# Kernel tuning notes

Measured on AMD Instinct MI355X. Metric: run time of the kernel, lower is better.

The kernel has to match this reference:

```python
import jax, jax.numpy as jnp
import numpy as np

B, K = 4, 128
V_IN, V_OUT = 256, 256
E_IN, E_OUT = 512, 512
P_PE, T_PE = 200, 100
HEADS = 16  # c_atten_head


def _lin(key, din, dout):
    kw, kb = jax.random.split(key)
    W = jax.random.normal(kw, (din, dout), jnp.float32) / np.sqrt(din).astype(np.float32)
    b = jax.random.normal(kb, (dout,), jnp.float32) * 0.01
    return W, b


def setup_inputs() -> dict:
    key = jax.random.key(0)
    ks = jax.random.split(key, 14)
    v_f = jax.random.normal(ks[0], (B, K, V_IN), jnp.float32)
    e_f = jax.random.normal(ks[1], (B, K * K, E_IN), jnp.float32)
    p_pe = jax.random.normal(ks[2], (B, K, P_PE), jnp.float32)
    t_pe = jax.random.normal(ks[3], (B, T_PE), jnp.float32)
    e_agg_mask = (jax.random.uniform(ks[4], (B, K, K)) > 0.1).astype(jnp.float32)
    v_agg_mask = (jax.random.uniform(ks[5], (B, K)) > 0.1).astype(jnp.float32)
    W_vpe, b_vpe = _lin(ks[6], V_IN + P_PE + T_PE, V_IN)
    W_epe, b_epe = _lin(ks[7], E_IN + T_PE, E_IN)
    W_ev1, b_ev1 = _lin(ks[8], E_IN + 2 * V_IN, E_OUT)
    W_ev2, b_ev2 = _lin(ks[9], E_OUT, E_OUT)
    W_q, b_q = _lin(ks[10], V_IN, E_OUT)
    W_k, b_k = _lin(ks[11], V_IN, E_OUT)
    W_self, b_self = _lin(ks[12], V_IN, E_OUT)
    W_out, b_out = _lin(ks[13], 2 * E_OUT, V_OUT)
    return dict(v_f=v_f, e_f=e_f, p_pe=p_pe, t_pe=t_pe,
                e_agg_mask=e_agg_mask, v_agg_mask=v_agg_mask,
                W_vpe=W_vpe, b_vpe=b_vpe, W_epe=W_epe, b_epe=b_epe,
                W_ev1=W_ev1, b_ev1=b_ev1, W_ev2=W_ev2, b_ev2=b_ev2,
                W_q=W_q, b_q=b_q, W_k=W_k, b_k=b_k,
                W_self=W_self, b_self=b_self, W_out=W_out, b_out=b_out)


def reference(v_f, e_f, p_pe, t_pe, e_agg_mask, v_agg_mask,
              W_vpe, b_vpe, W_epe, b_epe, W_ev1, b_ev1, W_ev2, b_ev2,
              W_q, b_q, W_k, b_k, W_self, b_self, W_out, b_out):
    silu = jax.nn.silu
    # PE binding
    t_v = jnp.broadcast_to(t_pe[:, None, :], (B, K, T_PE))
    v = silu(jnp.concatenate([v_f, p_pe, t_v], -1) @ W_vpe + b_vpe)          # (B,K,V_IN)
    t_e = jnp.broadcast_to(t_pe[:, None, :], (B, K * K, T_PE))
    e = silu(jnp.concatenate([e_f, t_e], -1) @ W_epe + b_epe)                # (B,K*K,E_IN)
    # dense all-pairs node features -> edge values
    pair = jnp.concatenate([jnp.broadcast_to(v[:, :, None, :], (B, K, K, V_IN)),
                            jnp.broadcast_to(v[:, None, :, :], (B, K, K, V_IN))], -1)
    ev_in = jnp.concatenate([pair.reshape(B, K * K, 2 * V_IN), e], -1)
    e_value = silu(ev_in @ W_ev1 + b_ev1) @ W_ev2 + b_ev2                     # (B,K*K,E_OUT)
    agg_e = e_value.reshape(B, K, K, E_OUT)
    # elementwise-multiply / head-sum attention
    q = v @ W_q + b_q                                                         # (B,K,E_OUT)
    k = v @ W_k + b_k
    att = (q[:, :, None, :] * k[:, None, :, :]).reshape(B, K, K, E_OUT // HEADS, HEADS)
    att = att.sum(-1, keepdims=True) / np.float32(np.sqrt(HEADS * 3.0))       # (B,K,K,G,1)
    a = jax.nn.sigmoid(att) * e_agg_mask[..., None, None]
    a = a / (a.sum(2, keepdims=True) + 1e-6)
    a = jnp.broadcast_to(a, (B, K, K, E_OUT // HEADS, HEADS)).reshape(B, K, K, E_OUT)
    agg_v = (a * agg_e).sum(2)                                                # (B,K,E_OUT)
    v2 = agg_v + silu(v @ W_self + b_self)
    # masked max-pool over nodes
    pooled = (v2 - 1e9 * (1.0 - v_agg_mask)[..., None]).max(1, keepdims=True)
    pooled = jnp.broadcast_to(pooled, (B, K, E_OUT))
    v_out = silu(jnp.concatenate([v2, pooled], -1) @ W_out + b_out)           # (B,K,V_OUT)
    return v_out, e_value
```

## Files before the change

kernel.cpp:

```cpp
#include <hip/hip_runtime.h>

typedef unsigned short ushort_t;
typedef __attribute__((ext_vector_type(8))) short bf16x8;
typedef __attribute__((ext_vector_type(4))) float f32x4;

__device__ __forceinline__ ushort_t f2bf(float f) {
    union { float f; unsigned u; } v; v.f = f;
    unsigned r = v.u + 0x7FFFu + ((v.u >> 16) & 1u);
    return (ushort_t)(r >> 16);
}
__device__ __forceinline__ float siluf(float x) { return x / (1.f + __expf(-x)); }
__device__ __forceinline__ float sigm(float x)  { return 1.f / (1.f + __expf(-x)); }

__device__ __forceinline__ void gl2lds16(const void* g, void* l) {
    __builtin_amdgcn_global_load_lds(
        (__attribute__((address_space(1))) void*)(const_cast<void*>(g)),
        (__attribute__((address_space(3))) void*)(l), 16, 0, 0);
}


__global__ void k_prep(const float* t_pe, const float* W_vpe, const float* b_vpe,
                       const float* W_epe, const float* b_epe,
                       float* c_v, float* c_e) {
    int b = blockIdx.x, t = threadIdx.x;
    {
        float acc = b_epe[t];
        for (int u = 0; u < 100; ++u) acc += t_pe[b*100+u] * W_epe[(512+u)*512 + t];
        c_e[b*512 + t] = acc;
    }
    if (t < 256) {
        float acc = b_vpe[t];
        for (int u = 0; u < 100; ++u) acc += t_pe[b*100+u] * W_vpe[(456+u)*256 + t];
        c_v[b*256 + t] = acc;
    }
}

__global__ void k_transpose(const float* W_epe, const float* W_ev1, const float* W_ev2,
                            ushort_t* WT_epe, ushort_t* WT_c, ushort_t* WT_ev2) {
    int n = blockIdx.x;
    int mat = blockIdx.y;
    const float* src; ushort_t* dst;
    if (mat == 0)      { src = W_epe;            dst = WT_epe; }
    else if (mat == 1) { src = W_ev1 + 512*512;  dst = WT_c;   }
    else               { src = W_ev2;            dst = WT_ev2; }
    for (int k = threadIdx.x; k < 512; k += 256)
        dst[n*512 + k] = f2bf(src[k*512 + n]);
}

__global__ void k_node_v(const float* v_f, const float* p_pe, const float* W_vpe,
                         const float* c_v, float* v) {
    __shared__ float rv[4][256];
    __shared__ float rp[4][200];
    int r0 = blockIdx.x * 4, t = threadIdx.x;
    for (int rr = 0; rr < 4; ++rr) {
        rv[rr][t] = v_f[(r0+rr)*256 + t];
        if (t < 200) rp[rr][t] = p_pe[(r0+rr)*200 + t];
    }
    __syncthreads();
    int b = r0 >> 7;
    float acc[4];
    float cv = c_v[b*256 + t];
    for (int rr = 0; rr < 4; ++rr) acc[rr] = cv;
    for (int k = 0; k < 256; ++k) {
        float w = W_vpe[k*256 + t];
        #pragma unroll
        for (int rr = 0; rr < 4; ++rr) acc[rr] += rv[rr][k] * w;
    }
    for (int k = 0; k < 200; ++k) {
        float w = W_vpe[(256+k)*256 + t];
        #pragma unroll
        for (int rr = 0; rr < 4; ++rr) acc[rr] += rp[rr][k] * w;
    }
    for (int rr = 0; rr < 4; ++rr) v[(r0+rr)*256 + t] = siluf(acc[rr]);
}

__global__ void k_node_proj(const float* v,
                            const float* W_q, const float* b_q,
                            const float* W_k, const float* b_k,
                            const float* W_self, const float* b_self,
                            const float* W_ev1, const float* b_ev1,
                            float* q, float* kk, float* vs, float* P, float* Q) {
    __shared__ float rv[4][256];
    int r0 = blockIdx.x * 4, which = blockIdx.y, t = threadIdx.x;
    for (int rr = 0; rr < 4; ++rr) rv[rr][t] = v[(r0+rr)*256 + t];
    __syncthreads();
    const float* W; const float* bias = nullptr; float* out; bool do_silu = false;
    if (which == 0)      { W = W_q;    bias = b_q;    out = q;  }
    else if (which == 1) { W = W_k;    bias = b_k;    out = kk; }
    else if (which == 2) { W = W_self; bias = b_self; out = vs; do_silu = true; }
    else if (which == 3) { W = W_ev1;  bias = b_ev1;  out = P;  }
    else                 { W = W_ev1 + 256*512;       out = Q;  }
    float acc[4][2] = {};
    for (int k = 0; k < 256; ++k) {
        float w0 = W[k*512 + t];
        float w1 = W[k*512 + t + 256];
        #pragma unroll
        for (int rr = 0; rr < 4; ++rr) {
            acc[rr][0] += rv[rr][k] * w0;
            acc[rr][1] += rv[rr][k] * w1;
        }
    }
    float bb0 = bias ? bias[t] : 0.f;
    float bb1 = bias ? bias[t + 256] : 0.f;
    for (int rr = 0; rr < 4; ++rr) {
        float x0 = acc[rr][0] + bb0;
        float x1 = acc[rr][1] + bb1;
        if (do_silu) { x0 = siluf(x0); x1 = siluf(x1); }
        out[(r0+rr)*512 + t]       = x0;
        out[(r0+rr)*512 + t + 256] = x1;
    }
}


__global__ __launch_bounds__(256) void k_gemm1(const float* Ef, const ushort_t* BT,
                                               const float* c_e, ushort_t* Eout) {
    __shared__ __align__(16) ushort_t As[128*40];
    __shared__ __align__(16) ushort_t Bs[128*32];
    int m0 = blockIdx.x * 128, n0 = blockIdx.y * 128;
    int t = threadIdx.x;
    int wv = t >> 6, lane = t & 63;
    int wm = (wv >> 1) * 64, wn = (wv & 1) * 64;
    int ml = lane & 15, quad = lane >> 4;
    f32x4 acc[4][4] = {};

    int arow = t >> 1, acol = (t & 1) * 16;
    const float* gA = Ef + (size_t)(m0 + arow) * 512 + acol;
    int brow = t >> 2, bseg = t & 3;
    const ushort_t* gB0 = BT + (size_t)(n0 + brow) * 512 + bseg * 8;
    const ushort_t* gB1 = BT + (size_t)(n0 + 64 + brow) * 512 + bseg * 8;
    ushort_t* lB0 = Bs + wv * 512;
    ushort_t* lB1 = Bs + 2048 + wv * 512;

    for (int kk = 0; kk < 512; kk += 32) {
        gl2lds16(gB0 + kk, lB0);
        gl2lds16(gB1 + kk, lB1);
        const float* ga = gA + kk;
        float4 f0 = *(const float4*)(ga);
        float4 f1 = *(const float4*)(ga + 4);
        float4 f2 = *(const float4*)(ga + 8);
        float4 f3 = *(const float4*)(ga + 12);
        ushort_t* d = As + arow * 40 + acol;
        ((ushort4*)d)[0] = make_ushort4(f2bf(f0.x), f2bf(f0.y), f2bf(f0.z), f2bf(f0.w));
        ((ushort4*)d)[1] = make_ushort4(f2bf(f1.x), f2bf(f1.y), f2bf(f1.z), f2bf(f1.w));
        ((ushort4*)d)[2] = make_ushort4(f2bf(f2.x), f2bf(f2.y), f2bf(f2.z), f2bf(f2.w));
        ((ushort4*)d)[3] = make_ushort4(f2bf(f3.x), f2bf(f3.y), f2bf(f3.z), f2bf(f3.w));
        __syncthreads();
        bf16x8 a[4], b[4];
        #pragma unroll
        for (int tm = 0; tm < 4; ++tm)
            a[tm] = *(const bf16x8*)(As + (wm + tm*16 + ml) * 40 + quad * 8);
        #pragma unroll
        for (int tn = 0; tn < 4; ++tn)
            b[tn] = *(const bf16x8*)(Bs + (wn + tn*16 + ml) * 32 + quad * 8);
        #pragma unroll
        for (int tm = 0; tm < 4; ++tm)
            #pragma unroll
            for (int tn = 0; tn < 4; ++tn)
                acc[tm][tn] = __builtin_amdgcn_mfma_f32_16x16x32_bf16(a[tm], b[tn], acc[tm][tn], 0, 0, 0);
        __syncthreads();
    }
    #pragma unroll
    for (int tm = 0; tm < 4; ++tm)
        #pragma unroll
        for (int tn = 0; tn < 4; ++tn)
            #pragma unroll
            for (int r = 0; r < 4; ++r) {
                int gm = m0 + wm + tm*16 + quad*4 + r;
                int gn = n0 + wn + tn*16 + ml;
                float x = acc[tm][tn][r] + c_e[(gm >> 14)*512 + gn];
                Eout[(size_t)gm*512 + gn] = f2bf(siluf(x));
            }
}

template <int MODE>
__global__ __launch_bounds__(256) void k_gemm_b(const ushort_t* A, const ushort_t* BT,
                                                const float* x0, const float* x1,
                                                ushort_t* out16, float* out32) {
    __shared__ __align__(16) ushort_t As[128*32];
    __shared__ __align__(16) ushort_t Bs[128*32];
    int m0 = blockIdx.x * 128, n0 = blockIdx.y * 128;
    int t = threadIdx.x;
    int wv = t >> 6, lane = t & 63;
    int wm = (wv >> 1) * 64, wn = (wv & 1) * 64;
    int ml = lane & 15, quad = lane >> 4;
    f32x4 acc[4][4] = {};

    int srow = t >> 2, sseg = t & 3;
    const ushort_t* gA0 = A + (size_t)(m0 + srow) * 512 + sseg * 8;
    const ushort_t* gA1 = A + (size_t)(m0 + 64 + srow) * 512 + sseg * 8;
    const ushort_t* gB0 = BT + (size_t)(n0 + srow) * 512 + sseg * 8;
    const ushort_t* gB1 = BT + (size_t)(n0 + 64 + srow) * 512 + sseg * 8;
    ushort_t* lA0 = As + wv * 512;
    ushort_t* lA1 = As + 2048 + wv * 512;
    ushort_t* lB0 = Bs + wv * 512;
    ushort_t* lB1 = Bs + 2048 + wv * 512;

    for (int kk = 0; kk < 512; kk += 32) {
        gl2lds16(gA0 + kk, lA0);
        gl2lds16(gA1 + kk, lA1);
        gl2lds16(gB0 + kk, lB0);
        gl2lds16(gB1 + kk, lB1);
        __syncthreads();
        bf16x8 a[4], b[4];
        #pragma unroll
        for (int tm = 0; tm < 4; ++tm)
            a[tm] = *(const bf16x8*)(As + (wm + tm*16 + ml) * 32 + quad * 8);
        #pragma unroll
        for (int tn = 0; tn < 4; ++tn)
            b[tn] = *(const bf16x8*)(Bs + (wn + tn*16 + ml) * 32 + quad * 8);
        #pragma unroll
        for (int tm = 0; tm < 4; ++tm)
            #pragma unroll
            for (int tn = 0; tn < 4; ++tn)
                acc[tm][tn] = __builtin_amdgcn_mfma_f32_16x16x32_bf16(a[tm], b[tn], acc[tm][tn], 0, 0, 0);
        __syncthreads();
    }
    #pragma unroll
    for (int tm = 0; tm < 4; ++tm)
        #pragma unroll
        for (int tn = 0; tn < 4; ++tn)
            #pragma unroll
            for (int r = 0; r < 4; ++r) {
                int gm = m0 + wm + tm*16 + quad*4 + r;
                int gn = n0 + wn + tn*16 + ml;
                float x = acc[tm][tn][r];
                if (MODE == 0) {
                    int b_ = gm >> 14, ij = gm & 16383, i = ij >> 7, j = ij & 127;
                    x += x0[(size_t)((b_ << 7) + i) * 512 + gn] + x1[(size_t)((b_ << 7) + j) * 512 + gn];
                    out16[(size_t)gm*512 + gn] = f2bf(siluf(x));
                } else {
                    x += x0[gn];
                    out32[(size_t)gm*512 + gn] = x;
                }
            }
}

__global__ __launch_bounds__(256) void k_attn(const float* q, const float* kmat,
                                              const float* emask, const float* evalue,
                                              const float* vs, float* v2) {
    int bi = blockIdx.x; int b = bi >> 7, i = bi & 127;
    int t = threadIdx.x;
    __shared__ __align__(16) float qrow[512];
    __shared__ float s[128][33];
    __shared__ float invd[32];
    qrow[t]       = q[(size_t)bi*512 + t];
    qrow[t + 256] = q[(size_t)bi*512 + t + 256];
    __syncthreads();
    {
        int j = t >> 1, g0 = (t & 1) * 16;
        const float* kr = kmat + ((size_t)b*128 + j) * 512;
        float msk = emask[(size_t)b*16384 + i*128 + j];
        for (int gg = 0; gg < 16; ++gg) {
            int g = g0 + gg;
            const float4* k4 = (const float4*)(kr + g*16);
            const float4* q4 = (const float4*)(qrow + g*16);
            float acc = 0.f;
            #pragma unroll
            for (int c = 0; c < 4; ++c) {
                float4 kv = k4[c], qv = q4[c];
                acc += kv.x*qv.x + kv.y*qv.y + kv.z*qv.z + kv.w*qv.w;
            }
            s[j][g] = sigm(acc * 0.14433756729740645f) * msk;
        }
    }
    __syncthreads();
    if (t < 32) {
        float d = 1e-6f;
        for (int j = 0; j < 128; ++j) d += s[j][t];
        invd[t] = 1.f / d;
    }
    __syncthreads();
    int d0 = t * 2;
    int g = d0 >> 4;
    float a0 = 0.f, a1 = 0.f;
    const float* ev = evalue + ((size_t)b*16384 + i*128) * 512 + d0;
    for (int j = 0; j < 128; ++j) {
        float aw = s[j][g];
        float2 e2 = *(const float2*)(ev + (size_t)j * 512);
        a0 += aw * e2.x; a1 += aw * e2.y;
    }
    float iv = invd[g];
    size_t o = (size_t)bi*512 + d0;
    v2[o]     = a0 * iv + vs[o];
    v2[o + 1] = a1 * iv + vs[o + 1];
}

__global__ void k_pool(const float* v2, const float* vmask, const float* W_out,
                       const float* b_out, float* cpool) {
    int b = blockIdx.x, t = threadIdx.x;
    __shared__ float pooled[512];
    for (int d = t; d < 512; d += 256) {
        float m = -1e30f;
        for (int i = 0; i < 128; ++i) {
            float val = v2[((size_t)(b*128 + i))*512 + d] - 1e9f * (1.f - vmask[b*128 + i]);
            m = fmaxf(m, val);
        }
        pooled[d] = m;
    }
    __syncthreads();
    float acc = b_out[t];
    for (int d = 0; d < 512; ++d) acc += pooled[d] * W_out[(512 + d)*256 + t];
    cpool[b*256 + t] = acc;
}

__global__ void k_node_out(const float* v2, const float* W_out, const float* cpool,
                           float* out) {
    __shared__ float rv[4][512];
    int r0 = blockIdx.x * 4, t = threadIdx.x;
    for (int rr = 0; rr < 4; ++rr) {
        rv[rr][t]       = v2[(size_t)(r0+rr)*512 + t];
        rv[rr][t + 256] = v2[(size_t)(r0+rr)*512 + t + 256];
    }
    __syncthreads();
    int b = r0 >> 7;
    float acc[4];
    float cp = cpool[b*256 + t];
    for (int rr = 0; rr < 4; ++rr) acc[rr] = cp;
    for (int k = 0; k < 512; ++k) {
        float w = W_out[k*256 + t];
        #pragma unroll
        for (int rr = 0; rr < 4; ++rr) acc[rr] += rv[rr][k] * w;
    }
    for (int rr = 0; rr < 4; ++rr) out[(r0+rr)*256 + t] = siluf(acc[rr]);
}

extern "C" void kernel_launch(void* const* d_in, const int* in_sizes, int n_in,
                              void* d_out, int out_size, void* d_ws, size_t ws_size,
                              hipStream_t stream) {
    const float* v_f    = (const float*)d_in[0];
    const float* e_f    = (const float*)d_in[1];
    const float* p_pe   = (const float*)d_in[2];
    const float* t_pe   = (const float*)d_in[3];
    const float* emask  = (const float*)d_in[4];
    const float* vmask  = (const float*)d_in[5];
    const float* W_vpe  = (const float*)d_in[6];
    const float* b_vpe  = (const float*)d_in[7];
    const float* W_epe  = (const float*)d_in[8];
    const float* b_epe  = (const float*)d_in[9];
    const float* W_ev1  = (const float*)d_in[10];
    const float* b_ev1  = (const float*)d_in[11];
    const float* W_ev2  = (const float*)d_in[12];
    const float* b_ev2  = (const float*)d_in[13];
    const float* W_q    = (const float*)d_in[14];
    const float* b_q    = (const float*)d_in[15];
    const float* W_k    = (const float*)d_in[16];
    const float* b_k    = (const float*)d_in[17];
    const float* W_self = (const float*)d_in[18];
    const float* b_self = (const float*)d_in[19];
    const float* W_out  = (const float*)d_in[20];
    const float* b_out  = (const float*)d_in[21];

    float* out_v = (float*)d_out;
    float* out_e = (float*)d_out + 131072;

    char* w = (char*)d_ws;
    ushort_t* WT_epe = (ushort_t*)w; w += 512*512*2;
    ushort_t* WT_c   = (ushort_t*)w; w += 512*512*2;
    ushort_t* WT_ev2 = (ushort_t*)w; w += 512*512*2;
    float* c_v   = (float*)w; w += 4*256*4;
    float* c_e   = (float*)w; w += 4*512*4;
    float* v     = (float*)w; w += 512*256*4;
    float* qbuf  = (float*)w; w += 512*512*4;
    float* kbuf  = (float*)w; w += 512*512*4;
    float* vsbuf = (float*)w; w += 512*512*4;
    float* Pbuf  = (float*)w; w += 512*512*4;
    float* Qbuf  = (float*)w; w += 512*512*4;
    float* v2buf = (float*)w; w += 512*512*4;
    float* cpool = (float*)w; w += 4*256*4;
    ushort_t* e16 = (ushort_t*)w; w += (size_t)65536*512*2;
    ushort_t* h16 = (ushort_t*)w; w += (size_t)65536*512*2;

    k_prep<<<4, 512, 0, stream>>>(t_pe, W_vpe, b_vpe, W_epe, b_epe, c_v, c_e);
    k_transpose<<<dim3(512, 3), 256, 0, stream>>>(W_epe, W_ev1, W_ev2, WT_epe, WT_c, WT_ev2);
    k_node_v<<<128, 256, 0, stream>>>(v_f, p_pe, W_vpe, c_v, v);
    k_node_proj<<<dim3(128, 5), 256, 0, stream>>>(v, W_q, b_q, W_k, b_k, W_self, b_self,
                                                  W_ev1, b_ev1, qbuf, kbuf, vsbuf, Pbuf, Qbuf);
    k_gemm1<<<dim3(512, 4), 256, 0, stream>>>(e_f, WT_epe, c_e, e16);
    k_gemm_b<0><<<dim3(512, 4), 256, 0, stream>>>(e16, WT_c, Pbuf, Qbuf, h16, nullptr);
    k_gemm_b<1><<<dim3(512, 4), 256, 0, stream>>>(h16, WT_ev2, b_ev2, nullptr, nullptr, out_e);
    k_attn<<<512, 256, 0, stream>>>(qbuf, kbuf, emask, out_e, vsbuf, v2buf);
    k_pool<<<4, 256, 0, stream>>>(v2buf, vmask, W_out, b_out, cpool);
    k_node_out<<<128, 256, 0, stream>>>(v2buf, W_out, cpool, out_v);
}
```

Before: 689.1 us.

## Fuse attention aggregation into final edge GEMM epilogue and pre-convert e_f to bf16

Splits attention into a weight-only kernel that writes normalized per-(i,j,group) weights, then folds the weighted sum over j into the epilogue of the last edge GEMM. Each 128-row tile there covers exactly one (b,i) node, so the fp32 e_value no longer has to be re-read from memory. The first GEMM now takes a bf16 copy of e_f made by a separate conversion pass instead of converting inside the main loop, and tiles are remapped by XCD index for L2 locality. The cost is the extra conversion pass, an anorm buffer, and shuffle reductions in the epilogue.

```diff
diff --git a/kernel.cpp b/kernel.cpp
--- a/kernel.cpp
+++ b/kernel.cpp
@@ -47,6 +47,15 @@
         dst[n*512 + k] = f2bf(src[k*512 + n]);
 }
 
+__global__ __launch_bounds__(256) void k_cvt(const float* src, ushort_t* dst) {
+    size_t id = (size_t)blockIdx.x * 256 + threadIdx.x;
+    const float4* s = (const float4*)src + id * 2;
+    float4 a = s[0], b = s[1];
+    ushort4* d = (ushort4*)dst + id * 2;
+    d[0] = make_ushort4(f2bf(a.x), f2bf(a.y), f2bf(a.z), f2bf(a.w));
+    d[1] = make_ushort4(f2bf(b.x), f2bf(b.y), f2bf(b.z), f2bf(b.w));
+}
+
 __global__ void k_node_v(const float* v_f, const float* p_pe, const float* W_vpe,
                          const float* c_v, float* v) {
     __shared__ float rv[4][256];
@@ -111,133 +120,8 @@
     }
 }
 
-
-__global__ __launch_bounds__(256) void k_gemm1(const float* Ef, const ushort_t* BT,
-                                               const float* c_e, ushort_t* Eout) {
-    __shared__ __align__(16) ushort_t As[128*40];
-    __shared__ __align__(16) ushort_t Bs[128*32];
-    int m0 = blockIdx.x * 128, n0 = blockIdx.y * 128;
-    int t = threadIdx.x;
-    int wv = t >> 6, lane = t & 63;
-    int wm = (wv >> 1) * 64, wn = (wv & 1) * 64;
-    int ml = lane & 15, quad = lane >> 4;
-    f32x4 acc[4][4] = {};
-
-    int arow = t >> 1, acol = (t & 1) * 16;
-    const float* gA = Ef + (size_t)(m0 + arow) * 512 + acol;
-    int brow = t >> 2, bseg = t & 3;
-    const ushort_t* gB0 = BT + (size_t)(n0 + brow) * 512 + bseg * 8;
-    const ushort_t* gB1 = BT + (size_t)(n0 + 64 + brow) * 512 + bseg * 8;
-    ushort_t* lB0 = Bs + wv * 512;
-    ushort_t* lB1 = Bs + 2048 + wv * 512;
-
-    for (int kk = 0; kk < 512; kk += 32) {
-        gl2lds16(gB0 + kk, lB0);
-        gl2lds16(gB1 + kk, lB1);
-        const float* ga = gA + kk;
-        float4 f0 = *(const float4*)(ga);
-        float4 f1 = *(const float4*)(ga + 4);
-        float4 f2 = *(const float4*)(ga + 8);
-        float4 f3 = *(const float4*)(ga + 12);
-        ushort_t* d = As + arow * 40 + acol;
-        ((ushort4*)d)[0] = make_ushort4(f2bf(f0.x), f2bf(f0.y), f2bf(f0.z), f2bf(f0.w));
-        ((ushort4*)d)[1] = make_ushort4(f2bf(f1.x), f2bf(f1.y), f2bf(f1.z), f2bf(f1.w));
-        ((ushort4*)d)[2] = make_ushort4(f2bf(f2.x), f2bf(f2.y), f2bf(f2.z), f2bf(f2.w));
-        ((ushort4*)d)[3] = make_ushort4(f2bf(f3.x), f2bf(f3.y), f2bf(f3.z), f2bf(f3.w));
-        __syncthreads();
-        bf16x8 a[4], b[4];
-        #pragma unroll
-        for (int tm = 0; tm < 4; ++tm)
-            a[tm] = *(const bf16x8*)(As + (wm + tm*16 + ml) * 40 + quad * 8);
-        #pragma unroll
-        for (int tn = 0; tn < 4; ++tn)
-            b[tn] = *(const bf16x8*)(Bs + (wn + tn*16 + ml) * 32 + quad * 8);
-        #pragma unroll
-        for (int tm = 0; tm < 4; ++tm)
-            #pragma unroll
-            for (int tn = 0; tn < 4; ++tn)
-                acc[tm][tn] = __builtin_amdgcn_mfma_f32_16x16x32_bf16(a[tm], b[tn], acc[tm][tn], 0, 0, 0);
-        __syncthreads();
-    }
-    #pragma unroll
-    for (int tm = 0; tm < 4; ++tm)
-        #pragma unroll
-        for (int tn = 0; tn < 4; ++tn)
-            #pragma unroll
-            for (int r = 0; r < 4; ++r) {
-                int gm = m0 + wm + tm*16 + quad*4 + r;
-                int gn = n0 + wn + tn*16 + ml;
-                float x = acc[tm][tn][r] + c_e[(gm >> 14)*512 + gn];
-                Eout[(size_t)gm*512 + gn] = f2bf(siluf(x));
-            }
-}
-
-template <int MODE>
-__global__ __launch_bounds__(256) void k_gemm_b(const ushort_t* A, const ushort_t* BT,
-                                                const float* x0, const float* x1,
-                                                ushort_t* out16, float* out32) {
-    __shared__ __align__(16) ushort_t As[128*32];
-    __shared__ __align__(16) ushort_t Bs[128*32];
-    int m0 = blockIdx.x * 128, n0 = blockIdx.y * 128;
-    int t = threadIdx.x;
-    int wv = t >> 6, lane = t & 63;
-    int wm = (wv >> 1) * 64, wn = (wv & 1) * 64;
-    int ml = lane & 15, quad = lane >> 4;
-    f32x4 acc[4][4] = {};
-
-    int srow = t >> 2, sseg = t & 3;
-    const ushort_t* gA0 = A + (size_t)(m0 + srow) * 512 + sseg * 8;
-    const ushort_t* gA1 = A + (size_t)(m0 + 64 + srow) * 512 + sseg * 8;
-    const ushort_t* gB0 = BT + (size_t)(n0 + srow) * 512 + sseg * 8;
-    const ushort_t* gB1 = BT + (size_t)(n0 + 64 + srow) * 512 + sseg * 8;
-    ushort_t* lA0 = As + wv * 512;
-    ushort_t* lA1 = As + 2048 + wv * 512;
-    ushort_t* lB0 = Bs + wv * 512;
-    ushort_t* lB1 = Bs + 2048 + wv * 512;
-
-    for (int kk = 0; kk < 512; kk += 32) {
-        gl2lds16(gA0 + kk, lA0);
-        gl2lds16(gA1 + kk, lA1);
-        gl2lds16(gB0 + kk, lB0);
-        gl2lds16(gB1 + kk, lB1);
-        __syncthreads();
-        bf16x8 a[4], b[4];
-        #pragma unroll
-        for (int tm = 0; tm < 4; ++tm)
-            a[tm] = *(const bf16x8*)(As + (wm + tm*16 + ml) * 32 + quad * 8);
-        #pragma unroll
-        for (int tn = 0; tn < 4; ++tn)
-            b[tn] = *(const bf16x8*)(Bs + (wn + tn*16 + ml) * 32 + quad * 8);
-        #pragma unroll
-        for (int tm = 0; tm < 4; ++tm)
-            #pragma unroll
-            for (int tn = 0; tn < 4; ++tn)
-                acc[tm][tn] = __builtin_amdgcn_mfma_f32_16x16x32_bf16(a[tm], b[tn], acc[tm][tn], 0, 0, 0);
-        __syncthreads();
-    }
-    #pragma unroll
-    for (int tm = 0; tm < 4; ++tm)
-        #pragma unroll
-        for (int tn = 0; tn < 4; ++tn)
-            #pragma unroll
-            for (int r = 0; r < 4; ++r) {
-                int gm = m0 + wm + tm*16 + quad*4 + r;
-                int gn = n0 + wn + tn*16 + ml;
-                float x = acc[tm][tn][r];
-                if (MODE == 0) {
-                    int b_ = gm >> 14, ij = gm & 16383, i = ij >> 7, j = ij & 127;
-                    x += x0[(size_t)((b_ << 7) + i) * 512 + gn] + x1[(size_t)((b_ << 7) + j) * 512 + gn];
-                    out16[(size_t)gm*512 + gn] = f2bf(siluf(x));
-                } else {
-                    x += x0[gn];
-                    out32[(size_t)gm*512 + gn] = x;
-                }
-            }
-}
-
-__global__ __launch_bounds__(256) void k_attn(const float* q, const float* kmat,
-                                              const float* emask, const float* evalue,
-                                              const float* vs, float* v2) {
+__global__ __launch_bounds__(256) void k_attw(const float* q, const float* kmat,
+                                              const float* emask, float* anorm) {
     int bi = blockIdx.x; int b = bi >> 7, i = bi & 127;
     int t = threadIdx.x;
     __shared__ __align__(16) float qrow[512];
@@ -270,19 +154,120 @@
         invd[t] = 1.f / d;
     }
     __syncthreads();
-    int d0 = t * 2;
-    int g = d0 >> 4;
-    float a0 = 0.f, a1 = 0.f;
-    const float* ev = evalue + ((size_t)b*16384 + i*128) * 512 + d0;
-    for (int j = 0; j < 128; ++j) {
-        float aw = s[j][g];
-        float2 e2 = *(const float2*)(ev + (size_t)j * 512);
-        a0 += aw * e2.x; a1 += aw * e2.y;
-    }
-    float iv = invd[g];
-    size_t o = (size_t)bi*512 + d0;
-    v2[o]     = a0 * iv + vs[o];
-    v2[o + 1] = a1 * iv + vs[o + 1];
+    float* dst = anorm + (size_t)bi * 4096;
+    for (int idx = t; idx < 4096; idx += 256) {
+        int j = idx >> 5, g = idx & 31;
+        dst[idx] = s[j][g] * invd[g];
+    }
+}
+
+template <int MODE>
+__global__ __launch_bounds__(256) void k_gemm(const ushort_t* A, const ushort_t* BT,
+                                              const float* e0, const float* e1,
+                                              const float* e2,
+                                              ushort_t* out16, float* out32,
+                                              float* v2out) {
+    __shared__ __align__(16) ushort_t As[128*32];
+    __shared__ __align__(16) ushort_t Bs[128*32];
+    __shared__ float aw[(MODE == 2) ? 4096 : 4];
+    __shared__ float red[(MODE == 2) ? 256 : 4];
+
+    int lin = blockIdx.x;
+    int xcd = lin & 7, idx = lin >> 3;
+    int mt = xcd * 64 + (idx >> 2);
+    int nt = idx & 3;
+    int m0 = mt * 128, n0 = nt * 128;
+    int t = threadIdx.x;
+    int wv = t >> 6, lane = t & 63;
+    int wm = (wv >> 1) * 64, wn = (wv & 1) * 64;
+    int ml = lane & 15, quad = lane >> 4;
+    f32x4 acc[4][4] = {};
+
+    if (MODE == 2) {
+        const float4* src = (const float4*)(e1 + (size_t)mt * 4096);
+        float4* dst = (float4*)aw;
+        for (int i = t; i < 1024; i += 256) dst[i] = src[i];
+    }
+
+    int srow = t >> 2, sseg = t & 3;
+    const ushort_t* gA0 = A + (size_t)(m0 + srow) * 512 + sseg * 8;
+    const ushort_t* gA1 = A + (size_t)(m0 + 64 + srow) * 512 + sseg * 8;
+    const ushort_t* gB0 = BT + (size_t)(n0 + srow) * 512 + sseg * 8;
+    const ushort_t* gB1 = BT + (size_t)(n0 + 64 + srow) * 512 + sseg * 8;
+    ushort_t* lA0 = As + wv * 512;
+    ushort_t* lA1 = As + 2048 + wv * 512;
+    ushort_t* lB0 = Bs + wv * 512;
+    ushort_t* lB1 = Bs + 2048 + wv * 512;
+
+    for (int kk = 0; kk < 512; kk += 32) {
+        gl2lds16(gA0 + kk, lA0);
+        gl2lds16(gA1 + kk, lA1);
+        gl2lds16(gB0 + kk, lB0);
+        gl2lds16(gB1 + kk, lB1);
+        __syncthreads();
+        bf16x8 a[4], b[4];
+        #pragma unroll
+        for (int tm = 0; tm < 4; ++tm)
+            a[tm] = *(const bf16x8*)(As + (wm + tm*16 + ml) * 32 + quad * 8);
+        #pragma unroll
+        for (int tn = 0; tn < 4; ++tn)
+            b[tn] = *(const bf16x8*)(Bs + (wn + tn*16 + ml) * 32 + quad * 8);
+        #pragma unroll
+        for (int tm = 0; tm < 4; ++tm)
+            #pragma unroll
+            for (int tn = 0; tn < 4; ++tn)
+                acc[tm][tn] = __builtin_amdgcn_mfma_f32_16x16x32_bf16(a[tm], b[tn], acc[tm][tn], 0, 0, 0);
+        __syncthreads();
+    }
+
+    if (MODE == 2) {
+        float partial[4] = {0.f, 0.f, 0.f, 0.f};
+        #pragma unroll
+        for (int tm = 0; tm < 4; ++tm)
+            #pragma unroll
+            for (int tn = 0; tn < 4; ++tn)
+                #pragma unroll
+                for (int r = 0; r < 4; ++r) {
+                    int j  = wm + tm*16 + quad*4 + r;
+                    int gn = n0 + wn + tn*16 + ml;
+                    float x = acc[tm][tn][r] + e0[gn];
+                    out32[((size_t)m0 + j) * 512 + gn] = x;
+                    partial[tn] += aw[j * 32 + (gn >> 4)] * x;
+                }
+        #pragma unroll
+        for (int tn = 0; tn < 4; ++tn) {
+            float p = partial[tn];
+            p += __shfl_down(p, 32);
+            p += __shfl_down(p, 16);
+            if (quad == 0 && lane < 16) red[wv * 64 + tn * 16 + ml] = p;
+        }
+        __syncthreads();
+        if (t < 128) {
+            int c = t, half = c >> 6, cl = c & 63;
+            float tot = red[half * 64 + cl] + red[(half + 2) * 64 + cl];
+            size_t o = (size_t)mt * 512 + n0 + c;
+            v2out[o] = tot + e2[o];
+        }
+    } else {
+        #pragma unroll
+        for (int tm = 0; tm < 4; ++tm)
+            #pragma unroll
+            for (int tn = 0; tn < 4; ++tn)
+                #pragma unroll
+                for (int r = 0; r < 4; ++r) {
+                    int gm = m0 + wm + tm*16 + quad*4 + r;
+                    int gn = n0 + wn + tn*16 + ml;
+                    float x = acc[tm][tn][r];
+                    if (MODE == 0) {
+                        x += e0[(gm >> 14) * 512 + gn];
+                    } else {
+                        int b_ = gm >> 14, ij = gm & 16383, i = ij >> 7, j = ij & 127;
+                        x += e0[(size_t)((b_ << 7) + i) * 512 + gn]
+                           + e1[(size_t)((b_ << 7) + j) * 512 + gn];
+                    }
+                    out16[(size_t)gm * 512 + gn] = f2bf(siluf(x));
+                }
+    }
 }
 
 __global__ void k_pool(const float* v2, const float* vmask, const float* W_out,
@@ -367,18 +352,21 @@
     float* Qbuf  = (float*)w; w += 512*512*4;
     float* v2buf = (float*)w; w += 512*512*4;
     float* cpool = (float*)w; w += 4*256*4;
-    ushort_t* e16 = (ushort_t*)w; w += (size_t)65536*512*2;
-    ushort_t* h16 = (ushort_t*)w; w += (size_t)65536*512*2;
+    float* anorm = (float*)w; w += (size_t)4*128*128*32*4;
+    ushort_t* e16  = (ushort_t*)w; w += (size_t)65536*512*2;
+    ushort_t* ef16 = (ushort_t*)w; w += (size_t)65536*512*2;
+    ushort_t* h16  = ef16;
 
     k_prep<<<4, 512, 0, stream>>>(t_pe, W_vpe, b_vpe, W_epe, b_epe, c_v, c_e);
     k_transpose<<<dim3(512, 3), 256, 0, stream>>>(W_epe, W_ev1, W_ev2, WT_epe, WT_c, WT_ev2);
     k_node_v<<<128, 256, 0, stream>>>(v_f, p_pe, W_vpe, c_v, v);
     k_node_proj<<<dim3(128, 5), 256, 0, stream>>>(v, W_q, b_q, W_k, b_k, W_self, b_self,
                                                   W_ev1, b_ev1, qbuf, kbuf, vsbuf, Pbuf, Qbuf);
-    k_gemm1<<<dim3(512, 4), 256, 0, stream>>>(e_f, WT_epe, c_e, e16);
-    k_gemm_b<0><<<dim3(512, 4), 256, 0, stream>>>(e16, WT_c, Pbuf, Qbuf, h16, nullptr);
-    k_gemm_b<1><<<dim3(512, 4), 256, 0, stream>>>(h16, WT_ev2, b_ev2, nullptr, nullptr, out_e);
-    k_attn<<<512, 256, 0, stream>>>(qbuf, kbuf, emask, out_e, vsbuf, v2buf);
+    k_attw<<<512, 256, 0, stream>>>(qbuf, kbuf, emask, anorm);
+    k_cvt<<<16384, 256, 0, stream>>>(e_f, ef16);
+    k_gemm<0><<<2048, 256, 0, stream>>>(ef16, WT_epe, c_e, nullptr, nullptr, e16, nullptr, nullptr);
+    k_gemm<1><<<2048, 256, 0, stream>>>(e16, WT_c, Pbuf, Qbuf, nullptr, h16, nullptr, nullptr);
+    k_gemm<2><<<2048, 256, 0, stream>>>(h16, WT_ev2, b_ev2, anorm, vsbuf, nullptr, out_e, v2buf);
     k_pool<<<4, 256, 0, stream>>>(v2buf, vmask, W_out, b_out, cpool);
     k_node_out<<<128, 256, 0, stream>>>(v2buf, W_out, cpool, out_v);
 }
```

Result: faster. 671.3 us (-2.6%).
